# Performance work log

Hardware: AMD Instinct MI355X
Metric: run time of the kernel (lower is better)

Reference implementation:

```python
import jax, jax.numpy as jnp
import numpy as np

B, S, D, E, K = 4, 4096, 2048, 64, 2
LN_EPS = 1e-5
TEMP_EPS = 1e-6
Z_LOSS_COEF = 0.001
LB_COEF = 0.1


def setup_inputs() -> dict:
    key = jax.random.key(0)
    k1, k2 = jax.random.split(key)
    x = jax.random.normal(k1, (B, S, D), dtype=jnp.float32)
    # kaiming_normal fan_in (std = 1/sqrt(D)) scaled by 0.01, as in __init__
    W = jax.random.normal(k2, (E, D), dtype=jnp.float32) * jnp.float32(0.01 / np.sqrt(D))
    gamma = jnp.ones((E,), jnp.float32)   # LayerNorm weight
    beta = jnp.zeros((E,), jnp.float32)   # LayerNorm bias
    temperature = jnp.full((1,), 0.5, jnp.float32)
    return {"x": x, "W": W, "gamma": gamma, "beta": beta, "temperature": temperature}


def reference(x, W, gamma, beta, temperature):
    b, s, d = x.shape
    xf = x.reshape(-1, d)                                  # [N, D]
    logits = xf @ W.T                                      # [N, E]
    # LayerNorm over expert dim (biased variance, eps=1e-5, matches torch)
    mu = logits.mean(axis=-1, keepdims=True)
    var = jnp.mean(jnp.square(logits - mu), axis=-1, keepdims=True)
    logits = (logits - mu) * jax.lax.rsqrt(var + LN_EPS) * gamma + beta
    # temperature-scaled softmax
    routing_weights = jax.nn.softmax(logits / (temperature + TEMP_EPS), axis=-1)  # [N, E]
    # top-k + scatter into dense dispatch mask
    top_w, top_idx = jax.lax.top_k(routing_weights, K)     # [N, K]
    n = routing_weights.shape[0]
    dispatch = jnp.zeros_like(routing_weights).at[jnp.arange(n)[:, None], top_idx].set(top_w)
    dispatch = dispatch.reshape(b, s, E)                   # [B, S, E]
    # aux losses
    expert_load = dispatch.mean(axis=1)                    # [B, E]
    load_balance_loss = jnp.std(expert_load, ddof=1) / expert_load.mean() * 10.0
    router_z_loss = jnp.mean(jnp.square(logits))
    total_loss = ZLC * router_z_loss + LB_COEF * load_balance_loss if False else (
        Z_LOSS_COEF * router_z_loss + LB_COEF * load_balance_loss)
    return jax.lax.stop_gradient(routing_weights), dispatch, total_loss
```

## Files before the change

kernel.cpp:

```cpp
#include <hip/hip_runtime.h>
#include <hip/hip_bf16.h>
#include <float.h>
#include <math.h>

#define B_DIM 4
#define S_DIM 4096
#define D_DIM 2048
#define E_DIM 64
#define N_TOK 16384
#define TOKS 32
#define NBLK (N_TOK / TOKS)
#define NTHR 128
#define BK 64
#define LDK 72
#define KSTEPS (D_DIM / BK)
#define GAP_THRESH 1e-3f
#define MAXFLAG 16

typedef __bf16 bf16x8_t __attribute__((ext_vector_type(8)));
typedef float f32x4_t __attribute__((ext_vector_type(4)));

union U8 { bf16x8_t v; unsigned short u[8]; };

__device__ __forceinline__ void split2(float f, unsigned short& h, unsigned short& l) {
    unsigned int u = __float_as_uint(f);
    h = (unsigned short)(u >> 16);
    float hf = __uint_as_float(u & 0xFFFF0000u);
    l = (unsigned short)(__float_as_uint(f - hf) >> 16);
}

__global__ __launch_bounds__(NTHR, 2) void router_main(
    const float* __restrict__ x, const float* __restrict__ W,
    const float* __restrict__ gamma, const float* __restrict__ beta,
    const float* __restrict__ temperature,
    float* __restrict__ out_rw, float* __restrict__ out_dp,
    float* __restrict__ g_zsum, float* __restrict__ g_load)
{
    __shared__ unsigned short wh[2][E_DIM][LDK];
    __shared__ unsigned short wl[2][E_DIM][LDK];
    __shared__ float lgt[TOKS][E_DIM + 1];
    __shared__ float lgm[E_DIM], lbt[E_DIM], loadsum[E_DIM];
    __shared__ float smu[TOKS], srs[TOKS], sinv[TOKS];
    __shared__ int sel1[TOKS], sel2[TOKS];
    __shared__ int ftok[MAXFLAG], fcand[MAXFLAG][3];
    __shared__ int nflag;

    const int tid = threadIdx.x;
    const int tokBase = blockIdx.x * TOKS;
    const int lane = tid & 63;
    const int wv = tid >> 6;
    const int l15 = lane & 15;
    const int quad = lane >> 4;

    if (tid == 0) nflag = 0;
    if (tid < E_DIM) { lgm[tid] = gamma[tid]; lbt[tid] = beta[tid]; loadsum[tid] = 0.f; }

    const int rowW = tid >> 1;
    const int colW = (tid & 1) * 32;
    const float* wp = W + (size_t)rowW * D_DIM + colW;

    const float* xp = x + (size_t)(tokBase + wv * 16 + l15) * D_DIM + quad * 8;

    f32x4_t acc[4];
    #pragma unroll
    for (int t = 0; t < 4; ++t) acc[t] = (f32x4_t){0.f, 0.f, 0.f, 0.f};

    float4 wreg[8], xq[4], xn[4];
    #pragma unroll
    for (int j = 0; j < 8; ++j) wreg[j] = *(const float4*)(wp + j * 4);
    #pragma unroll
    for (int c = 0; c < 2; ++c) {
        xq[c * 2]     = *(const float4*)(xp + c * 32);
        xq[c * 2 + 1] = *(const float4*)(xp + c * 32 + 4);
    }
    #pragma unroll
    for (int j = 0; j < 8; ++j) {
        ushort4 h, l;
        split2(wreg[j].x, h.x, l.x); split2(wreg[j].y, h.y, l.y);
        split2(wreg[j].z, h.z, l.z); split2(wreg[j].w, h.w, l.w);
        *(ushort4*)&wh[0][rowW][colW + j * 4] = h;
        *(ushort4*)&wl[0][rowW][colW + j * 4] = l;
    }
    __syncthreads();

    for (int s = 0; s < KSTEPS; ++s) {
        const int cur = s & 1;
        const bool more = (s + 1 < KSTEPS);
        if (more) {
            const float* wq = wp + (s + 1) * BK;
            #pragma unroll
            for (int j = 0; j < 8; ++j) wreg[j] = *(const float4*)(wq + j * 4);
            const float* xg = xp + (s + 1) * BK;
            #pragma unroll
            for (int c = 0; c < 2; ++c) {
                xn[c * 2]     = *(const float4*)(xg + c * 32);
                xn[c * 2 + 1] = *(const float4*)(xg + c * 32 + 4);
            }
        }
        #pragma unroll
        for (int h = 0; h < 2; ++h) {
            float tf[8] = {xq[h*2].x, xq[h*2].y, xq[h*2].z, xq[h*2].w,
                           xq[h*2+1].x, xq[h*2+1].y, xq[h*2+1].z, xq[h*2+1].w};
            U8 ah, al;
            #pragma unroll
            for (int k = 0; k < 8; ++k) split2(tf[k], ah.u[k], al.u[k]);
            #pragma unroll
            for (int t = 0; t < 4; ++t) {
                U8 bh, bl;
                bh.v = *(const bf16x8_t*)&wh[cur][t * 16 + l15][h * 32 + quad * 8];
                bl.v = *(const bf16x8_t*)&wl[cur][t * 16 + l15][h * 32 + quad * 8];
                acc[t] = __builtin_amdgcn_mfma_f32_16x16x32_bf16(ah.v, bh.v, acc[t], 0, 0, 0);
                acc[t] = __builtin_amdgcn_mfma_f32_16x16x32_bf16(ah.v, bl.v, acc[t], 0, 0, 0);
                acc[t] = __builtin_amdgcn_mfma_f32_16x16x32_bf16(al.v, bh.v, acc[t], 0, 0, 0);
            }
        }
        if (more) {
            const int nxt = cur ^ 1;
            #pragma unroll
            for (int j = 0; j < 8; ++j) {
                ushort4 h, l;
                split2(wreg[j].x, h.x, l.x); split2(wreg[j].y, h.y, l.y);
                split2(wreg[j].z, h.z, l.z); split2(wreg[j].w, h.w, l.w);
                *(ushort4*)&wh[nxt][rowW][colW + j * 4] = h;
                *(ushort4*)&wl[nxt][rowW][colW + j * 4] = l;
            }
            #pragma unroll
            for (int j = 0; j < 4; ++j) xq[j] = xn[j];
        }
        __syncthreads();
    }

    #pragma unroll
    for (int t = 0; t < 4; ++t)
        #pragma unroll
        for (int r = 0; r < 4; ++r)
            lgt[wv * 16 + quad * 4 + r][t * 16 + l15] = acc[t][r];
    __syncthreads();

    const int tok = wv * 16 + l15;
    const int q = quad;
    const float it = 1.f / (temperature[0] + 1e-6f);
    float s1 = 0.f, s2 = 0.f;
    #pragma unroll
    for (int e = 0; e < 16; ++e) { float v = lgt[tok][q * 16 + e]; s1 += v; s2 += v * v; }
    s1 += __shfl_xor(s1, 16); s1 += __shfl_xor(s1, 32);
    s2 += __shfl_xor(s2, 16); s2 += __shfl_xor(s2, 32);
    const float mu  = s1 * (1.f / 64.f);
    const float var = s2 * (1.f / 64.f) - mu * mu;
    const float rs  = rsqrtf(var + 1e-5f);
    if (q == 0) { smu[tok] = mu; srs[tok] = rs; }

    float m0 = -FLT_MAX, m1 = -FLT_MAX, m2 = -FLT_MAX;
    int   i0 = -1, i1 = -1, i2 = -1;
    float zl = 0.f;
    #pragma unroll
    for (int e = 0; e < 16; ++e) {
        int c = q * 16 + e;
        float y = (lgt[tok][c] - mu) * rs * lgm[c] + lbt[c];
        lgt[tok][c] = y;
        zl += y * y;
        if (y > m0)      { m2 = m1; i2 = i1; m1 = m0; i1 = i0; m0 = y; i0 = c; }
        else if (y > m1) { m2 = m1; i2 = i1; m1 = y; i1 = c; }
        else if (y > m2) { m2 = y; i2 = c; }
    }
    #pragma unroll
    for (int d = 16; d <= 32; d <<= 1) {
        float n0 = __shfl_xor(m0, d), n1 = __shfl_xor(m1, d), n2 = __shfl_xor(m2, d);
        int   j0 = __shfl_xor(i0, d), j1 = __shfl_xor(i1, d), j2 = __shfl_xor(i2, d);
        bool t0 = (m0 > n0) || (m0 == n0 && i0 < j0);
        float r0v = t0 ? m0 : n0; int r0i = t0 ? i0 : j0;
        float A0v = t0 ? m1 : m0; int A0i = t0 ? i1 : i0;
        float A1v = t0 ? m2 : m1; int A1i = t0 ? i2 : i1;
        float B0v = t0 ? n0 : n1; int B0i = t0 ? j0 : j1;
        float B1v = t0 ? n1 : n2; int B1i = t0 ? j1 : j2;
        bool t1 = (A0v > B0v) || (A0v == B0v && A0i < B0i);
        float r1v = t1 ? A0v : B0v; int r1i = t1 ? A0i : B0i;
        float A0w = t1 ? A1v : A0v; int A0j = t1 ? A1i : A0i;
        float B0w = t1 ? B0v : B1v; int B0j = t1 ? B0i : B1i;
        bool t2 = (A0w > B0w) || (A0w == B0w && A0j < B0j);
        float r2v = t2 ? A0w : B0w; int r2i = t2 ? A0j : B0j;
        m0 = r0v; i0 = r0i; m1 = r1v; i1 = r1i; m2 = r2v; i2 = r2i;
    }
    if (q == 0) {
        sel1[tok] = i0; sel2[tok] = i1;
        if (m1 - m2 < GAP_THRESH) {
            int sf = atomicAdd(&nflag, 1);
            if (sf < MAXFLAG) { ftok[sf] = tok; fcand[sf][0] = i0; fcand[sf][1] = i1; fcand[sf][2] = i2; }
        }
    }
    float es = 0.f;
    #pragma unroll
    for (int e = 0; e < 16; ++e) {
        int c = q * 16 + e;
        float ev = __expf((lgt[tok][c] - m0) * it);
        lgt[tok][c] = ev; es += ev;
    }
    es += __shfl_xor(es, 16); es += __shfl_xor(es, 32);
    if (q == 0) sinv[tok] = 1.f / es;
    zl += __shfl_xor(zl, 1); zl += __shfl_xor(zl, 2); zl += __shfl_xor(zl, 4);
    zl += __shfl_xor(zl, 8); zl += __shfl_xor(zl, 16); zl += __shfl_xor(zl, 32);
    if (lane == 0) atomicAdd(g_zsum, zl);
    __syncthreads();

    const int nf = min(nflag, MAXFLAG);
    for (int f = wv; f < nf; f += 2) {
        const int tk = ftok[f];
        const int c0 = fcand[f][0], c1 = fcand[f][1], c2 = fcand[f][2];
        const float* xr = x + (size_t)(tokBase + tk) * D_DIM;
        const float* w0 = W + (size_t)c0 * D_DIM;
        const float* w1 = W + (size_t)c1 * D_DIM;
        const float* w2 = W + (size_t)c2 * D_DIM;
        double L0 = 0.0, L1 = 0.0, L2 = 0.0;
        for (int i = lane; i < D_DIM; i += 64) {
            double xv = (double)xr[i];
            L0 += xv * (double)w0[i];
            L1 += xv * (double)w1[i];
            L2 += xv * (double)w2[i];
        }
        #pragma unroll
        for (int off = 32; off; off >>= 1) {
            L0 += __shfl_down(L0, off);
            L1 += __shfl_down(L1, off);
            L2 += __shfl_down(L2, off);
        }
        if (lane == 0) {
            double dmu = (double)smu[tk], drs = (double)srs[tk];
            double y0 = (L0 - dmu) * drs * (double)lgm[c0] + (double)lbt[c0];
            double y1 = (L1 - dmu) * drs * (double)lgm[c1] + (double)lbt[c1];
            double y2 = (L2 - dmu) * drs * (double)lgm[c2] + (double)lbt[c2];
            bool g01 = (y0 > y1) || (y0 == y1 && c0 < c1);
            bool g02 = (y0 > y2) || (y0 == y2 && c0 < c2);
            bool g12 = (y1 > y2) || (y1 == y2 && c1 < c2);
            int a, b;
            if (!g01 && !g02)      { a = c1; b = c2; }
            else if (g01 && !g12)  { a = c0; b = c2; }
            else                   { a = c0; b = c1; }
            sel1[tk] = a; sel2[tk] = b;
        }
    }
    __syncthreads();

    if (tid < TOKS) {
        float inv = sinv[tid];
        atomicAdd(&loadsum[sel1[tid]], lgt[tid][sel1[tid]] * inv);
        atomicAdd(&loadsum[sel2[tid]], lgt[tid][sel2[tid]] * inv);
    }
    __syncthreads();
    if (tid < E_DIM) atomicAdd(&g_load[(tokBase >> 12) * E_DIM + tid], loadsum[tid]);

    float* orw = out_rw + (size_t)tokBase * E_DIM;
    float* odp = out_dp + (size_t)tokBase * E_DIM;
    for (int i = tid; i < TOKS * E_DIM; i += NTHR) {
        int r = i >> 6, c = i & 63;
        float p = lgt[r][c] * sinv[r];
        orw[i] = p;
        odp[i] = (c == sel1[r] || c == sel2[r]) ? p : 0.f;
    }
}

__global__ void router_fin(const float* __restrict__ ws, float* __restrict__ out_loss) {
    __shared__ float sv[B_DIM * E_DIM];
    const int tid = threadIdx.x;
    sv[tid] = ws[8 + tid] * (1.f / S_DIM);
    __syncthreads();
    if (tid == 0) {
        float s = 0.f;
        for (int i = 0; i < B_DIM * E_DIM; ++i) s += sv[i];
        const float mean = s * (1.f / (B_DIM * E_DIM));
        float ss = 0.f;
        for (int i = 0; i < B_DIM * E_DIM; ++i) { float d = sv[i] - mean; ss += d * d; }
        const float sd = sqrtf(ss * (1.f / (B_DIM * E_DIM - 1)));
        const float z = ws[0] * (1.f / ((float)N_TOK * E_DIM));
        out_loss[0] = 0.001f * z + 0.1f * (sd / mean) * 10.f;
    }
}

extern "C" void kernel_launch(void* const* d_in, const int* in_sizes, int n_in,
                              void* d_out, int out_size, void* d_ws, size_t ws_size,
                              hipStream_t stream) {
    const float* x     = (const float*)d_in[0];
    const float* W     = (const float*)d_in[1];
    const float* gamma = (const float*)d_in[2];
    const float* beta  = (const float*)d_in[3];
    const float* temp  = (const float*)d_in[4];
    float* out  = (float*)d_out;
    float* rw   = out;
    float* dp   = out + (size_t)N_TOK * E_DIM;
    float* loss = out + 2 * (size_t)N_TOK * E_DIM;
    float* ws   = (float*)d_ws;

    hipMemsetAsync(d_ws, 0, 512 * sizeof(float), stream);
    router_main<<<dim3(NBLK), dim3(NTHR), 0, stream>>>(x, W, gamma, beta, temp,
                                                       rw, dp, ws, ws + 8);
    router_fin<<<dim3(1), dim3(256), 0, stream>>>(ws, loss);
}
```

Before: 264.3 us.

## Split GEMM reduction dimension across four wave pairs with shared-memory partial sum

Raises the block from 2 to 8 waves. Each wave pair computes the 32x64 logits tile over one quarter of D, and the partial accumulators are summed through shared memory before the LayerNorm/softmax epilogue, which runs on only two waves. The intent is more in-flight loads and MFMA work per block to hide memory latency on a memory-bound GEMV-like problem. In exchange, the double-buffered W tile becomes single-buffered per slice, which adds an extra barrier per k-step, and the partial-sum reduction costs additional shared memory and a pass over it.

```diff
diff --git a/kernel.cpp b/kernel.cpp
--- a/kernel.cpp
+++ b/kernel.cpp
@@ -10,10 +10,12 @@
 #define N_TOK 16384
 #define TOKS 32
 #define NBLK (N_TOK / TOKS)
-#define NTHR 128
+#define NTHR 512
 #define BK 64
 #define LDK 72
-#define KSTEPS (D_DIM / BK)
+#define SLICES 4
+#define DSLICE (D_DIM / SLICES)
+#define KSTEPS (DSLICE / BK)
 #define GAP_THRESH 1e-3f
 #define MAXFLAG 16
 
@@ -29,16 +31,22 @@
     l = (unsigned short)(__float_as_uint(f - hf) >> 16);
 }
 
-__global__ __launch_bounds__(NTHR, 2) void router_main(
+__global__ __launch_bounds__(NTHR, 4) void router_main(
     const float* __restrict__ x, const float* __restrict__ W,
     const float* __restrict__ gamma, const float* __restrict__ beta,
     const float* __restrict__ temperature,
     float* __restrict__ out_rw, float* __restrict__ out_dp,
     float* __restrict__ g_zsum, float* __restrict__ g_load)
 {
-    __shared__ unsigned short wh[2][E_DIM][LDK];
-    __shared__ unsigned short wl[2][E_DIM][LDK];
-    __shared__ float lgt[TOKS][E_DIM + 1];
+    __shared__ __align__(16) unsigned char shraw[SLICES * 64 * LDK * 2 * 2];
+    typedef unsigned short WPlane[64][LDK];
+    WPlane* const wh = (WPlane*)shraw;
+    WPlane* const wl = (WPlane*)(shraw + SLICES * 64 * LDK * sizeof(unsigned short));
+    typedef float PartT[TOKS][E_DIM + 2];
+    PartT* const part = (PartT*)shraw;
+    float (* const lgt)[E_DIM + 1] =
+        (float (*)[E_DIM + 1])(shraw + SLICES * TOKS * (E_DIM + 2) * sizeof(float));
+
     __shared__ float lgm[E_DIM], lbt[E_DIM], loadsum[E_DIM];
     __shared__ float smu[TOKS], srs[TOKS], sinv[TOKS];
     __shared__ int sel1[TOKS], sel2[TOKS];
@@ -49,17 +57,20 @@
     const int tokBase = blockIdx.x * TOKS;
     const int lane = tid & 63;
     const int wv = tid >> 6;
+    const int g  = wv & 1;
+    const int sl = wv >> 1;
     const int l15 = lane & 15;
     const int quad = lane >> 4;
 
     if (tid == 0) nflag = 0;
     if (tid < E_DIM) { lgm[tid] = gamma[tid]; lbt[tid] = beta[tid]; loadsum[tid] = 0.f; }
 
-    const int rowW = tid >> 1;
+    const int sslice = tid >> 7;
+    const int rowW = (tid & 127) >> 1;
     const int colW = (tid & 1) * 32;
-    const float* wp = W + (size_t)rowW * D_DIM + colW;
-
-    const float* xp = x + (size_t)(tokBase + wv * 16 + l15) * D_DIM + quad * 8;
+    const float* wp = W + (size_t)rowW * D_DIM + sslice * DSLICE + colW;
+
+    const float* xp = x + (size_t)(tokBase + g * 16 + l15) * D_DIM + sl * DSLICE + quad * 8;
 
     f32x4_t acc[4];
     #pragma unroll
@@ -78,13 +89,12 @@
         ushort4 h, l;
         split2(wreg[j].x, h.x, l.x); split2(wreg[j].y, h.y, l.y);
         split2(wreg[j].z, h.z, l.z); split2(wreg[j].w, h.w, l.w);
-        *(ushort4*)&wh[0][rowW][colW + j * 4] = h;
-        *(ushort4*)&wl[0][rowW][colW + j * 4] = l;
+        *(ushort4*)&wh[sslice][rowW][colW + j * 4] = h;
+        *(ushort4*)&wl[sslice][rowW][colW + j * 4] = l;
     }
     __syncthreads();
 
     for (int s = 0; s < KSTEPS; ++s) {
-        const int cur = s & 1;
         const bool more = (s + 1 < KSTEPS);
         if (more) {
             const float* wq = wp + (s + 1) * BK;
@@ -107,103 +117,111 @@
             #pragma unroll
             for (int t = 0; t < 4; ++t) {
                 U8 bh, bl;
-                bh.v = *(const bf16x8_t*)&wh[cur][t * 16 + l15][h * 32 + quad * 8];
-                bl.v = *(const bf16x8_t*)&wl[cur][t * 16 + l15][h * 32 + quad * 8];
+                bh.v = *(const bf16x8_t*)&wh[sl][t * 16 + l15][h * 32 + quad * 8];
+                bl.v = *(const bf16x8_t*)&wl[sl][t * 16 + l15][h * 32 + quad * 8];
                 acc[t] = __builtin_amdgcn_mfma_f32_16x16x32_bf16(ah.v, bh.v, acc[t], 0, 0, 0);
                 acc[t] = __builtin_amdgcn_mfma_f32_16x16x32_bf16(ah.v, bl.v, acc[t], 0, 0, 0);
                 acc[t] = __builtin_amdgcn_mfma_f32_16x16x32_bf16(al.v, bh.v, acc[t], 0, 0, 0);
             }
         }
+        __syncthreads();
         if (more) {
-            const int nxt = cur ^ 1;
             #pragma unroll
             for (int j = 0; j < 8; ++j) {
                 ushort4 h, l;
                 split2(wreg[j].x, h.x, l.x); split2(wreg[j].y, h.y, l.y);
                 split2(wreg[j].z, h.z, l.z); split2(wreg[j].w, h.w, l.w);
-                *(ushort4*)&wh[nxt][rowW][colW + j * 4] = h;
-                *(ushort4*)&wl[nxt][rowW][colW + j * 4] = l;
+                *(ushort4*)&wh[sslice][rowW][colW + j * 4] = h;
+                *(ushort4*)&wl[sslice][rowW][colW + j * 4] = l;
             }
             #pragma unroll
             for (int j = 0; j < 4; ++j) xq[j] = xn[j];
-        }
-        __syncthreads();
+            __syncthreads();
+        }
     }
 
     #pragma unroll
     for (int t = 0; t < 4; ++t)
         #pragma unroll
         for (int r = 0; r < 4; ++r)
-            lgt[wv * 16 + quad * 4 + r][t * 16 + l15] = acc[t][r];
-    __syncthreads();
-
-    const int tok = wv * 16 + l15;
-    const int q = quad;
-    const float it = 1.f / (temperature[0] + 1e-6f);
-    float s1 = 0.f, s2 = 0.f;
-    #pragma unroll
-    for (int e = 0; e < 16; ++e) { float v = lgt[tok][q * 16 + e]; s1 += v; s2 += v * v; }
-    s1 += __shfl_xor(s1, 16); s1 += __shfl_xor(s1, 32);
-    s2 += __shfl_xor(s2, 16); s2 += __shfl_xor(s2, 32);
-    const float mu  = s1 * (1.f / 64.f);
-    const float var = s2 * (1.f / 64.f) - mu * mu;
-    const float rs  = rsqrtf(var + 1e-5f);
-    if (q == 0) { smu[tok] = mu; srs[tok] = rs; }
-
-    float m0 = -FLT_MAX, m1 = -FLT_MAX, m2 = -FLT_MAX;
-    int   i0 = -1, i1 = -1, i2 = -1;
-    float zl = 0.f;
-    #pragma unroll
-    for (int e = 0; e < 16; ++e) {
-        int c = q * 16 + e;
-        float y = (lgt[tok][c] - mu) * rs * lgm[c] + lbt[c];
-        lgt[tok][c] = y;
-        zl += y * y;
-        if (y > m0)      { m2 = m1; i2 = i1; m1 = m0; i1 = i0; m0 = y; i0 = c; }
-        else if (y > m1) { m2 = m1; i2 = i1; m1 = y; i1 = c; }
-        else if (y > m2) { m2 = y; i2 = c; }
-    }
-    #pragma unroll
-    for (int d = 16; d <= 32; d <<= 1) {
-        float n0 = __shfl_xor(m0, d), n1 = __shfl_xor(m1, d), n2 = __shfl_xor(m2, d);
-        int   j0 = __shfl_xor(i0, d), j1 = __shfl_xor(i1, d), j2 = __shfl_xor(i2, d);
-        bool t0 = (m0 > n0) || (m0 == n0 && i0 < j0);
-        float r0v = t0 ? m0 : n0; int r0i = t0 ? i0 : j0;
-        float A0v = t0 ? m1 : m0; int A0i = t0 ? i1 : i0;
-        float A1v = t0 ? m2 : m1; int A1i = t0 ? i2 : i1;
-        float B0v = t0 ? n0 : n1; int B0i = t0 ? j0 : j1;
-        float B1v = t0 ? n1 : n2; int B1i = t0 ? j1 : j2;
-        bool t1 = (A0v > B0v) || (A0v == B0v && A0i < B0i);
-        float r1v = t1 ? A0v : B0v; int r1i = t1 ? A0i : B0i;
-        float A0w = t1 ? A1v : A0v; int A0j = t1 ? A1i : A0i;
-        float B0w = t1 ? B0v : B1v; int B0j = t1 ? B0i : B1i;
-        bool t2 = (A0w > B0w) || (A0w == B0w && A0j < B0j);
-        float r2v = t2 ? A0w : B0w; int r2i = t2 ? A0j : B0j;
-        m0 = r0v; i0 = r0i; m1 = r1v; i1 = r1i; m2 = r2v; i2 = r2i;
-    }
-    if (q == 0) {
-        sel1[tok] = i0; sel2[tok] = i1;
-        if (m1 - m2 < GAP_THRESH) {
-            int sf = atomicAdd(&nflag, 1);
-            if (sf < MAXFLAG) { ftok[sf] = tok; fcand[sf][0] = i0; fcand[sf][1] = i1; fcand[sf][2] = i2; }
-        }
-    }
-    float es = 0.f;
-    #pragma unroll
-    for (int e = 0; e < 16; ++e) {
-        int c = q * 16 + e;
-        float ev = __expf((lgt[tok][c] - m0) * it);
-        lgt[tok][c] = ev; es += ev;
-    }
-    es += __shfl_xor(es, 16); es += __shfl_xor(es, 32);
-    if (q == 0) sinv[tok] = 1.f / es;
-    zl += __shfl_xor(zl, 1); zl += __shfl_xor(zl, 2); zl += __shfl_xor(zl, 4);
-    zl += __shfl_xor(zl, 8); zl += __shfl_xor(zl, 16); zl += __shfl_xor(zl, 32);
-    if (lane == 0) atomicAdd(g_zsum, zl);
+            part[sl][g * 16 + quad * 4 + r][t * 16 + l15] = acc[t][r];
+    __syncthreads();
+
+    for (int i = tid; i < TOKS * E_DIM; i += NTHR) {
+        int r = i >> 6, c = i & 63;
+        lgt[r][c] = (part[0][r][c] + part[1][r][c]) + (part[2][r][c] + part[3][r][c]);
+    }
+    __syncthreads();
+
+    if (wv < 2) {
+        const int tok = wv * 16 + l15;
+        const int q = quad;
+        const float it = 1.f / (temperature[0] + 1e-6f);
+        float s1 = 0.f, s2 = 0.f;
+        #pragma unroll
+        for (int e = 0; e < 16; ++e) { float v = lgt[tok][q * 16 + e]; s1 += v; s2 += v * v; }
+        s1 += __shfl_xor(s1, 16); s1 += __shfl_xor(s1, 32);
+        s2 += __shfl_xor(s2, 16); s2 += __shfl_xor(s2, 32);
+        const float mu  = s1 * (1.f / 64.f);
+        const float var = s2 * (1.f / 64.f) - mu * mu;
+        const float rs  = rsqrtf(var + 1e-5f);
+        if (q == 0) { smu[tok] = mu; srs[tok] = rs; }
+
+        float m0 = -FLT_MAX, m1 = -FLT_MAX, m2 = -FLT_MAX;
+        int   i0 = -1, i1 = -1, i2 = -1;
+        float zl = 0.f;
+        #pragma unroll
+        for (int e = 0; e < 16; ++e) {
+            int c = q * 16 + e;
+            float y = (lgt[tok][c] - mu) * rs * lgm[c] + lbt[c];
+            lgt[tok][c] = y;
+            zl += y * y;
+            if (y > m0)      { m2 = m1; i2 = i1; m1 = m0; i1 = i0; m0 = y; i0 = c; }
+            else if (y > m1) { m2 = m1; i2 = i1; m1 = y; i1 = c; }
+            else if (y > m2) { m2 = y; i2 = c; }
+        }
+        #pragma unroll
+        for (int d = 16; d <= 32; d <<= 1) {
+            float n0 = __shfl_xor(m0, d), n1 = __shfl_xor(m1, d), n2 = __shfl_xor(m2, d);
+            int   j0 = __shfl_xor(i0, d), j1 = __shfl_xor(i1, d), j2 = __shfl_xor(i2, d);
+            bool t0 = (m0 > n0) || (m0 == n0 && i0 < j0);
+            float r0v = t0 ? m0 : n0; int r0i = t0 ? i0 : j0;
+            float A0v = t0 ? m1 : m0; int A0i = t0 ? i1 : i0;
+            float A1v = t0 ? m2 : m1; int A1i = t0 ? i2 : i1;
+            float B0v = t0 ? n0 : n1; int B0i = t0 ? j0 : j1;
+            float B1v = t0 ? n1 : n2; int B1i = t0 ? j1 : j2;
+            bool t1 = (A0v > B0v) || (A0v == B0v && A0i < B0i);
+            float r1v = t1 ? A0v : B0v; int r1i = t1 ? A0i : B0i;
+            float A0w = t1 ? A1v : A0v; int A0j = t1 ? A1i : A0i;
+            float B0w = t1 ? B0v : B1v; int B0j = t1 ? B0i : B1i;
+            bool t2 = (A0w > B0w) || (A0w == B0w && A0j < B0j);
+            float r2v = t2 ? A0w : B0w; int r2i = t2 ? A0j : B0j;
+            m0 = r0v; i0 = r0i; m1 = r1v; i1 = r1i; m2 = r2v; i2 = r2i;
+        }
+        if (q == 0) {
+            sel1[tok] = i0; sel2[tok] = i1;
+            if (m1 - m2 < GAP_THRESH) {
+                int sf = atomicAdd(&nflag, 1);
+                if (sf < MAXFLAG) { ftok[sf] = tok; fcand[sf][0] = i0; fcand[sf][1] = i1; fcand[sf][2] = i2; }
+            }
+        }
+        float es = 0.f;
+        #pragma unroll
+        for (int e = 0; e < 16; ++e) {
+            int c = q * 16 + e;
+            float ev = __expf((lgt[tok][c] - m0) * it);
+            lgt[tok][c] = ev; es += ev;
+        }
+        es += __shfl_xor(es, 16); es += __shfl_xor(es, 32);
+        if (q == 0) sinv[tok] = 1.f / es;
+        zl += __shfl_xor(zl, 1); zl += __shfl_xor(zl, 2); zl += __shfl_xor(zl, 4);
+        zl += __shfl_xor(zl, 8); zl += __shfl_xor(zl, 16); zl += __shfl_xor(zl, 32);
+        if (lane == 0) atomicAdd(g_zsum, zl);
+    }
     __syncthreads();
 
     const int nf = min(nflag, MAXFLAG);
-    for (int f = wv; f < nf; f += 2) {
+    for (int f = wv; f < nf; f += 8) {
         const int tk = ftok[f];
         const int c0 = fcand[f][0], c1 = fcand[f][1], c2 = fcand[f][2];
         const float* xr = x + (size_t)(tokBase + tk) * D_DIM;
```

Result: faster. 236.1 us (-10.7%).
